# Performance work log

Hardware: AMD Instinct MI355X
Metric: run time of the kernel (lower is better)

## Reference

```python
import jax, jax.numpy as jnp
import numpy as np

EMBED = 64
HEADS = 8
DHEAD = EMBED // HEADS  # 8
LAYERS = 4
VOCAB = 32000
SEQ = 1024
BATCH = 8
EPS = 1e-5


def setup_inputs() -> dict:
    key = jax.random.key(0)
    ks = jax.random.split(key, 24)
    s = 0.02
    inp = {
        "x": jax.random.randint(ks[0], (BATCH, SEQ), 0, VOCAB),
        "targets": jax.random.randint(ks[1], (BATCH, SEQ), 0, VOCAB),
        "tok_emb": jax.random.normal(ks[2], (VOCAB, EMBED)) * s,
        "pos_emb": jax.random.normal(ks[3], (SEQ, EMBED)) * s,
        # per-layer, per-head q/k/v projections (stored as (in,out) so y = x @ W + b)
        "Wq": jax.random.normal(ks[4], (LAYERS, HEADS, EMBED, DHEAD)) * s,
        "bq": jax.random.normal(ks[5], (LAYERS, HEADS, DHEAD)) * s,
        "Wk": jax.random.normal(ks[6], (LAYERS, HEADS, EMBED, DHEAD)) * s,
        "bk": jax.random.normal(ks[7], (LAYERS, HEADS, DHEAD)) * s,
        "Wv": jax.random.normal(ks[8], (LAYERS, HEADS, EMBED, DHEAD)) * s,
        "bv": jax.random.normal(ks[9], (LAYERS, HEADS, DHEAD)) * s,
        "ln1_g": jnp.ones((LAYERS, EMBED)) + jax.random.normal(ks[10], (LAYERS, EMBED)) * s,
        "ln1_b": jax.random.normal(ks[11], (LAYERS, EMBED)) * s,
        "ln2_g": jnp.ones((LAYERS, EMBED)) + jax.random.normal(ks[12], (LAYERS, EMBED)) * s,
        "ln2_b": jax.random.normal(ks[13], (LAYERS, EMBED)) * s,
        "W1": jax.random.normal(ks[14], (LAYERS, EMBED, 4 * EMBED)) * s,
        "b1": jax.random.normal(ks[15], (LAYERS, 4 * EMBED)) * s,
        "W2": jax.random.normal(ks[16], (LAYERS, 4 * EMBED, EMBED)) * s,
        "b2": jax.random.normal(ks[17], (LAYERS, EMBED)) * s,
        "Wout": jax.random.normal(ks[18], (EMBED, VOCAB)) * s,
        "bout": jax.random.normal(ks[19], (VOCAB,)) * s,
    }
    return inp


def _layernorm(x, g, b):
    mu = jnp.mean(x, axis=-1, keepdims=True)
    var = jnp.var(x, axis=-1, keepdims=True)
    return (x - mu) / jnp.sqrt(var + EPS) * g + b


def _mha(h, Wq, bq, Wk, bk, Wv, bv):
    B, T, C = h.shape
    q = jnp.einsum('btc,hcd->bhtd', h, Wq) + bq[:, None, :]
    k = jnp.einsum('btc,hcd->bhtd', h, Wk) + bk[:, None, :]
    v = jnp.einsum('btc,hcd->bhtd', h, Wv) + bv[:, None, :]
    # FAITHFUL to source: key output is .view(B, C, T) -- a raw reshape, not transpose
    kr = k.reshape(B, HEADS, DHEAD, T)
    w = jnp.einsum('bhtd,bhds->bhts', q, kr)  # [B,H,T,T]
    w = jnp.tril(w)
    w = jnp.where(w == 0, -jnp.inf, w)
    w = jax.nn.softmax(w / np.sqrt(DHEAD), axis=-1)
    o = jnp.einsum('bhts,bhsd->bhtd', w, v)
    return o.transpose(0, 2, 1, 3).reshape(B, T, HEADS * DHEAD)


def _forward(x, targets, tok_emb, pos_emb, Wq, bq, Wk, bk, Wv, bv,
             ln1_g, ln1_b, ln2_g, ln2_b, W1, b1, W2, b2, Wout, bout):
    B, T = x.shape
    h = tok_emb[x] + pos_emb[:T]
    for l in range(LAYERS):
        h = h + _layernorm(_mha(h, Wq[l], bq[l], Wk[l], bk[l], Wv[l], bv[l]), ln1_g[l], ln1_b[l])
        z = _layernorm(h, ln2_g[l], ln2_b[l])
        h = h + jax.nn.relu(z @ W1[l] + b1[l]) @ W2[l] + b2[l]
    logits = h @ Wout + bout  # [B,T,V]
    lp = jax.nn.log_softmax(logits.reshape(B * T, -1), axis=-1)
    nll = -jnp.take_along_axis(lp, targets.reshape(B * T, 1), axis=1)
    loss = jnp.mean(nll)
    return logits, loss


def reference(x, targets, tok_emb, pos_emb, Wq, bq, Wk, bk, Wv, bv,
              ln1_g, ln1_b, ln2_g, ln2_b, W1, b1, W2, b2, Wout, bout):
    return _forward(x, targets, tok_emb, pos_emb, Wq, bq, Wk, bk, Wv, bv,
                    ln1_g, ln1_b, ln2_g, ln2_b, W1, b1, W2, b2, Wout, bout)
```

## Files before the change

kernel.cpp:

```cpp
#include <hip/hip_runtime.h>
#include <hip/hip_bf16.h>
#include <math.h>

#define BB 8
#define TT 1024
#define CC 64
#define HH 8
#define DH 8
#define NLAY 4
#define VV 32000
#define FF 256
#define NR (BB*TT)
#define NLOGIT 262144000
#define NCB 125

typedef unsigned short u16;
typedef __attribute__((ext_vector_type(8))) short short8v;
typedef __attribute__((ext_vector_type(4))) float f32x4;

__device__ __forceinline__ float b2f(u16 u){
  union { float f; unsigned int i; } c; c.i = ((unsigned int)u) << 16; return c.f;
}
__device__ __forceinline__ u16 f2b(float f){
  union { float f; unsigned int i; } c; c.f = f;
  unsigned int x = c.i;
  return (u16)((x + 0x7FFF + ((x >> 16) & 1)) >> 16);
}

__global__ void k_probe(const void* ln1g, int* flag){
  if (threadIdx.x == 0 && blockIdx.x == 0){
    const u16* p = (const u16*)ln1g;
    int cnt = 0;
    for (int i = 0; i < 256; i++){ if ((p[i] >> 8) == 0x3F) cnt++; }
    *flag = (cnt > 192) ? 1 : 0;
  }
}

struct ConvArgs {
  const void* src[18];
  float* dst[18];
  int n[18];
  int blkoff[19];
  const int* flag;
  u16* wout16;
};
__global__ void k_convert(ConvArgs a){
  int isb = *a.flag;
  int bid = blockIdx.x;
  int t = 0;
  while (bid >= a.blkoff[t + 1]) t++;
  int base = (bid - a.blkoff[t]) * 1024 + threadIdx.x;
  const u16* s16 = (const u16*)a.src[t];
  const float* s32 = (const float*)a.src[t];
  float* d = a.dst[t];
  int n = a.n[t];
  #pragma unroll
  for (int e = 0; e < 4; e++){
    int i = base + e * 256;
    if (i < n){
      float v = isb ? b2f(s16[i]) : s32[i];
      d[i] = v;
      if (t == 16) a.wout16[i] = f2b(v);
    }
  }
}

__global__ void k_embed(const int* __restrict__ x, const float* __restrict__ tok,
                        const float* __restrict__ pos, float* __restrict__ h){
  int i = blockIdx.x * 256 + threadIdx.x;
  int r = i >> 6, c = i & 63;
  int t = r & (TT - 1);
  h[i] = tok[x[r] * 64 + c] + pos[t * 64 + c];
}

__global__ void k_qkv(const float* __restrict__ h,
                      const float* __restrict__ wq, const float* __restrict__ bq,
                      const float* __restrict__ wk, const float* __restrict__ bk,
                      const float* __restrict__ wv, const float* __restrict__ bv,
                      float* __restrict__ q, float* __restrict__ kp, float* __restrict__ vv){
  __shared__ float hs[4][64];
  int tid = threadIdx.x;
  int row0 = blockIdx.x * 4;
  hs[tid >> 6][tid & 63] = h[row0 * 64 + tid];
  __syncthreads();
  int rr = tid >> 6, o = tid & 63;
  int head = o >> 3, d = o & 7;
  int row = row0 + rr;
  int b = row >> 10, t = row & (TT - 1);
  float aq = bq[head * 8 + d], ak = bk[head * 8 + d], av = bv[head * 8 + d];
  #pragma unroll
  for (int c = 0; c < 64; c++){
    float hv = hs[rr][c];
    aq += hv * wq[(head * 64 + c) * 8 + d];
    ak += hv * wk[(head * 64 + c) * 8 + d];
    av += hv * wv[(head * 64 + c) * 8 + d];
  }
  int bh = b * HH + head;
  q[(bh * TT + t) * 8 + d] = aq;
  int i = t * 8 + d;
  kp[(bh * TT + (i & 1023)) * 8 + (i >> 10)] = ak;
  vv[(bh * TT + t) * 8 + d] = av;
}

__global__ void k_attn(const float* __restrict__ q, const float* __restrict__ kp,
                       const float* __restrict__ vv, float* __restrict__ att){
  __shared__ float qs[64][8], ks[64][8], vs[64][8];
  __shared__ float2 ml[256];
  __shared__ float po[256][8];
  int tid = threadIdx.x;
  int bh = blockIdx.y;
  int t0 = blockIdx.x * 64;
  const float* qb = q + (bh * TT + t0) * 8;
  for (int idx = tid; idx < 512; idx += 256) ((float*)qs)[idx] = qb[idx];
  __syncthreads();
  int tr = tid >> 2, pp = tid & 3;
  int t = t0 + tr;
  float qr[8];
  #pragma unroll
  for (int d = 0; d < 8; d++) qr[d] = qs[tr][d];
  float m = -1e30f, l = 0.f;
  float o[8] = {0,0,0,0,0,0,0,0};
  int ntile = blockIdx.x + 1;
  for (int st = 0; st < ntile; st++){
    int s0 = st * 64;
    __syncthreads();
    const float* kb = kp + (bh * TT + s0) * 8;
    const float* vb = vv + (bh * TT + s0) * 8;
    for (int idx = tid; idx < 512; idx += 256){
      ((float*)ks)[idx] = kb[idx];
      ((float*)vs)[idx] = vb[idx];
    }
    __syncthreads();
    float sc[16];
    float tm = -1e30f;
    #pragma unroll
    for (int j = 0; j < 16; j++){
      int si = pp + j * 4;
      int s = s0 + si;
      float acc = 0.f;
      #pragma unroll
      for (int d = 0; d < 8; d++) acc += qr[d] * ks[si][d];
      sc[j] = (s <= t) ? acc * 0.35355339059327378f : -1e30f;
      tm = fmaxf(tm, sc[j]);
    }
    float mn = fmaxf(m, tm);
    float fac = __expf(m - mn);
    l *= fac;
    #pragma unroll
    for (int d = 0; d < 8; d++) o[d] *= fac;
    #pragma unroll
    for (int j = 0; j < 16; j++){
      if (sc[j] > -0.9e30f){
        float e = __expf(sc[j] - mn);
        l += e;
        int si = pp + j * 4;
        #pragma unroll
        for (int d = 0; d < 8; d++) o[d] += e * vs[si][d];
      }
    }
    m = mn;
  }
  ml[tid] = make_float2(m, l);
  #pragma unroll
  for (int d = 0; d < 8; d++) po[tid][d] = o[d];
  __syncthreads();
  if (pp == 0){
    float M = -1e30f;
    #pragma unroll
    for (int p2 = 0; p2 < 4; p2++) M = fmaxf(M, ml[tid + p2].x);
    float L = 0.f;
    float O[8] = {0,0,0,0,0,0,0,0};
    #pragma unroll
    for (int p2 = 0; p2 < 4; p2++){
      float w = __expf(ml[tid + p2].x - M);
      L += ml[tid + p2].y * w;
      #pragma unroll
      for (int d = 0; d < 8; d++) O[d] += po[tid + p2][d] * w;
    }
    float inv = 1.f / L;
    int b = bh >> 3, hh = bh & 7;
    float* op = att + (b * TT + t) * 64 + hh * 8;
    #pragma unroll
    for (int d = 0; d < 8; d++) op[d] = O[d] * inv;
  }
}

__global__ void k_lnres(const float* __restrict__ src, const float* __restrict__ g,
                        const float* __restrict__ bb, float* __restrict__ h){
  int tid = threadIdx.x;
  int row = blockIdx.x * 4 + (tid >> 6);
  int lane = tid & 63;
  float x = src[row * 64 + lane];
  float s = x, sq = x * x;
  for (int msk = 32; msk; msk >>= 1){
    s += __shfl_xor(s, msk, 64);
    sq += __shfl_xor(sq, msk, 64);
  }
  float mu = s * (1.f / 64);
  float var = sq * (1.f / 64) - mu * mu;
  float rstd = rsqrtf(fmaxf(var, 0.f) + 1e-5f);
  h[row * 64 + lane] += (x - mu) * rstd * g[lane] + bb[lane];
}

__global__ void k_ffn(float* __restrict__ h, const float* __restrict__ g, const float* __restrict__ bb,
                      const float* __restrict__ w1, const float* __restrict__ b1,
                      const float* __restrict__ w2, const float* __restrict__ b2){
  __shared__ float z[8][64];
  __shared__ float a[8][256];
  int tid = threadIdx.x;
  int row0 = blockIdx.x * 8;
  {
    int rr = tid >> 5, cp = tid & 31;
    int c0 = cp * 2;
    const float* hp = h + (row0 + rr) * 64;
    float x0 = hp[c0], x1 = hp[c0 + 1];
    float s = x0 + x1, sq = x0 * x0 + x1 * x1;
    for (int msk = 16; msk; msk >>= 1){
      s += __shfl_xor(s, msk, 64);
      sq += __shfl_xor(sq, msk, 64);
    }
    float mu = s * (1.f / 64);
    float var = sq * (1.f / 64) - mu * mu;
    float rstd = rsqrtf(fmaxf(var, 0.f) + 1e-5f);
    z[rr][c0]     = (x0 - mu) * rstd * g[c0] + bb[c0];
    z[rr][c0 + 1] = (x1 - mu) * rstd * g[c0 + 1] + bb[c0 + 1];
  }
  __syncthreads();
  {
    int j = tid;
    float acc[8];
    float bj = b1[j];
    #pragma unroll
    for (int r = 0; r < 8; r++) acc[r] = bj;
    for (int c = 0; c < 64; c++){
      float w = w1[c * 256 + j];
      #pragma unroll
      for (int r = 0; r < 8; r++) acc[r] += z[r][c] * w;
    }
    #pragma unroll
    for (int r = 0; r < 8; r++) a[r][j] = fmaxf(acc[r], 0.f);
  }
  __syncthreads();
  #pragma unroll
  for (int half = 0; half < 2; half++){
    int oi = tid + half * 256;
    int r = oi >> 6, c = oi & 63;
    float acc = b2[c];
    for (int k = 0; k < 256; k++) acc += a[r][k] * w2[k * 64 + c];
    h[(row0 + r) * 64 + c] += acc;
  }
}

__global__ void k_h2b(const float* __restrict__ h, u16* __restrict__ hb){
  int i = blockIdx.x * 256 + threadIdx.x;
  hb[i] = f2b(h[i]);
}

__global__ void __launch_bounds__(256) k_logits(const u16* __restrict__ hb, const u16* __restrict__ wb,
                                                const float* __restrict__ bout, float* __restrict__ logits,
                                                float2* __restrict__ part){
  int tid = threadIdx.x;
  int wave = tid >> 6, lane = tid & 63;
  int lr = lane & 15, lg = lane >> 4;
  int row0 = blockIdx.y * 64;
  int colw = blockIdx.x * 256 + wave * 64;

  short8v af[4][2];
  #pragma unroll
  for (int mi = 0; mi < 4; mi++)
    #pragma unroll
    for (int kk = 0; kk < 2; kk++)
      af[mi][kk] = *(const short8v*)(hb + (row0 + mi * 16 + lr) * 64 + kk * 32 + lg * 8);

  short8v bf[4][2];
  #pragma unroll
  for (int nf = 0; nf < 4; nf++){
    int col = colw + nf * 16 + lr;
    #pragma unroll
    for (int kk = 0; kk < 2; kk++){
      #pragma unroll
      for (int i = 0; i < 8; i++)
        bf[nf][kk][i] = (short)wb[(kk * 32 + lg * 8 + i) * VV + col];
    }
  }

  f32x4 acc[4][4];
  #pragma unroll
  for (int mi = 0; mi < 4; mi++)
    #pragma unroll
    for (int nf = 0; nf < 4; nf++)
      acc[mi][nf] = (f32x4){0.f, 0.f, 0.f, 0.f};

  #pragma unroll
  for (int mi = 0; mi < 4; mi++){
    #pragma unroll
    for (int nf = 0; nf < 4; nf++){
      acc[mi][nf] = __builtin_amdgcn_mfma_f32_16x16x32_bf16(af[mi][0], bf[nf][0], acc[mi][nf], 0, 0, 0);
      acc[mi][nf] = __builtin_amdgcn_mfma_f32_16x16x32_bf16(af[mi][1], bf[nf][1], acc[mi][nf], 0, 0, 0);
    }
  }

  float bo[4];
  #pragma unroll
  for (int nf = 0; nf < 4; nf++) bo[nf] = bout[colw + nf * 16 + lr];

  #pragma unroll
  for (int mi = 0; mi < 4; mi++){
    #pragma unroll
    for (int nf = 0; nf < 4; nf++){
      int colg = colw + nf * 16 + lr;
      #pragma unroll
      for (int r = 0; r < 4; r++){
        int rowg = row0 + mi * 16 + lg * 4 + r;
        logits[(size_t)rowg * VV + colg] = acc[mi][nf][r] + bo[nf];
      }
    }
  }

  __shared__ float2 wml[4][64];
  #pragma unroll
  for (int mi = 0; mi < 4; mi++){
    #pragma unroll
    for (int r = 0; r < 4; r++){
      float v0 = acc[mi][0][r] + bo[0], v1 = acc[mi][1][r] + bo[1];
      float v2 = acc[mi][2][r] + bo[2], v3 = acc[mi][3][r] + bo[3];
      float mx = fmaxf(fmaxf(v0, v1), fmaxf(v2, v3));
      for (int msk = 1; msk < 16; msk <<= 1) mx = fmaxf(mx, __shfl_xor(mx, msk, 64));
      float sume = __expf(v0 - mx) + __expf(v1 - mx) + __expf(v2 - mx) + __expf(v3 - mx);
      for (int msk = 1; msk < 16; msk <<= 1) sume += __shfl_xor(sume, msk, 64);
      if (lr == 0) wml[wave][mi * 16 + lg * 4 + r] = make_float2(mx, sume);
    }
  }
  __syncthreads();
  if (tid < 64){
    float M = -1e30f;
    #pragma unroll
    for (int w = 0; w < 4; w++) M = fmaxf(M, wml[w][tid].x);
    float L = 0.f;
    #pragma unroll
    for (int w = 0; w < 4; w++){
      float2 p = wml[w][tid];
      L += p.y * __expf(p.x - M);
    }
    part[(size_t)blockIdx.x * NR + row0 + tid] = make_float2(M, L);
  }
}

__global__ void k_loss(const float2* __restrict__ part, const float* __restrict__ logits,
                       const int* __restrict__ tgt, float* __restrict__ lpart){
  int row = blockIdx.x * 256 + threadIdx.x;
  float M = -1e30f;
  for (int j = 0; j < NCB; j++) M = fmaxf(M, part[(size_t)j * NR + row].x);
  float L = 0.f;
  for (int j = 0; j < NCB; j++){
    float2 p = part[(size_t)j * NR + row];
    L += p.y * __expf(p.x - M);
  }
  float lse = M + __logf(L);
  float tl = logits[(size_t)row * VV + tgt[row]];
  float nll = lse - tl;
  __shared__ float red[4];
  for (int msk = 32; msk; msk >>= 1) nll += __shfl_xor(nll, msk, 64);
  if ((threadIdx.x & 63) == 0) red[threadIdx.x >> 6] = nll;
  __syncthreads();
  if (threadIdx.x == 0) lpart[blockIdx.x] = red[0] + red[1] + red[2] + red[3];
}
__global__ void k_loss2(const float* __restrict__ lpart, float* __restrict__ out){
  if (threadIdx.x == 0 && blockIdx.x == 0){
    float s = 0.f;
    for (int i = 0; i < 32; i++) s += lpart[i];
    out[NLOGIT] = s * (1.f / NR);
  }
}

extern "C" void kernel_launch(void* const* d_in, const int* in_sizes, int n_in,
                              void* d_out, int out_size, void* d_ws, size_t ws_size,
                              hipStream_t stream){
  (void)in_sizes; (void)n_in; (void)out_size; (void)ws_size;
  const int* x = (const int*)d_in[0];
  const int* targets = (const int*)d_in[1];
  float* out = (float*)d_out;

  static const int WN[18] = {2048000, 65536, 16384, 256, 16384, 256, 16384, 256,
                             256, 256, 256, 256, 65536, 1024, 65536, 256, 2048000, 32000};
  char* ws = (char*)d_ws;
  size_t off = 0;
  auto alloc = [&](size_t bytes) -> void* {
    void* p = ws + off;
    off += (bytes + 255) & ~(size_t)255;
    return p;
  };
  int* flag = (int*)alloc(256);
  float* wf[18];
  for (int i = 0; i < 18; i++) wf[i] = (float*)alloc((size_t)WN[i] * 4);
  float* h     = (float*)alloc((size_t)NR * 64 * 4);
  float* q     = (float*)alloc((size_t)NR * 64 * 4);
  float* kp    = (float*)alloc((size_t)NR * 64 * 4);
  float* v     = (float*)alloc((size_t)NR * 64 * 4);
  float* att_o = (float*)alloc((size_t)NR * 64 * 4);
  u16* hb      = (u16*)alloc((size_t)NR * 64 * 2);
  u16* wout16  = (u16*)alloc((size_t)2048000 * 2);
  float2* part = (float2*)alloc((size_t)NCB * NR * 8);
  float* lpart = (float*)alloc(32 * 4);

  hipLaunchKernelGGL(k_probe, dim3(1), dim3(64), 0, stream, d_in[10], flag);
  ConvArgs ca;
  int blk = 0;
  for (int i = 0; i < 18; i++){
    ca.src[i] = d_in[2 + i];
    ca.dst[i] = wf[i];
    ca.n[i] = WN[i];
    ca.blkoff[i] = blk;
    blk += (WN[i] + 1023) / 1024;
  }
  ca.blkoff[18] = blk;
  ca.flag = flag;
  ca.wout16 = wout16;
  hipLaunchKernelGGL(k_convert, dim3(blk), dim3(256), 0, stream, ca);

  hipLaunchKernelGGL(k_embed, dim3(2048), dim3(256), 0, stream, x, wf[0], wf[1], h);

  for (int l = 0; l < NLAY; l++){
    hipLaunchKernelGGL(k_qkv, dim3(2048), dim3(256), 0, stream, h,
                       wf[2] + l * 4096, wf[3] + l * 64,
                       wf[4] + l * 4096, wf[5] + l * 64,
                       wf[6] + l * 4096, wf[7] + l * 64,
                       q, kp, v);
    hipLaunchKernelGGL(k_attn, dim3(16, 64), dim3(256), 0, stream, q, kp, v, att_o);
    hipLaunchKernelGGL(k_lnres, dim3(2048), dim3(256), 0, stream, att_o,
                       wf[8] + l * 64, wf[9] + l * 64, h);
    hipLaunchKernelGGL(k_ffn, dim3(1024), dim3(256), 0, stream, h,
                       wf[10] + l * 64, wf[11] + l * 64,
                       wf[12] + l * 16384, wf[13] + l * 256,
                       wf[14] + l * 16384, wf[15] + l * 64);
  }

  hipLaunchKernelGGL(k_h2b, dim3(2048), dim3(256), 0, stream, h, hb);
  hipLaunchKernelGGL(k_logits, dim3(NCB, 128), dim3(256), 0, stream, hb, wout16, wf[17], out, part);
  hipLaunchKernelGGL(k_loss, dim3(32), dim3(256), 0, stream, part, out, targets, lpart);
  hipLaunchKernelGGL(k_loss2, dim3(1), dim3(64), 0, stream, lpart, out);
}
```

Before: 825.2 us.

## Rewrite attention with bf16 MFMA and transpose Wout for vectorized B loads

Attention is rewritten as one-wave blocks of 16 query rows. QK^T and PV are computed with bf16 16x16x32 MFMA instructions over 32-key chunks, with an online softmax done through cross-lane shuffles. Q (pre-scaled), K and a transposed V are now stored in bf16 by the QKV kernel, which halves their memory traffic. Wout is also stored transposed in bf16, so the logits kernel loads B fragments as 16-byte vectors instead of strided scalar loads. In exchange, attention scores and probabilities lose precision in bf16, and only 8 of the 32 K dimension slots in the MFMA are used.

```diff
diff --git a/kernel.cpp b/kernel.cpp
--- a/kernel.cpp
+++ b/kernel.cpp
@@ -15,16 +15,20 @@
 #define NCB 125
 
 typedef unsigned short u16;
+typedef unsigned int u32;
 typedef __attribute__((ext_vector_type(8))) short short8v;
 typedef __attribute__((ext_vector_type(4))) float f32x4;
 
 __device__ __forceinline__ float b2f(u16 u){
-  union { float f; unsigned int i; } c; c.i = ((unsigned int)u) << 16; return c.f;
+  union { float f; u32 i; } c; c.i = ((u32)u) << 16; return c.f;
 }
 __device__ __forceinline__ u16 f2b(float f){
-  union { float f; unsigned int i; } c; c.f = f;
-  unsigned int x = c.i;
+  union { float f; u32 i; } c; c.f = f;
+  u32 x = c.i;
   return (u16)((x + 0x7FFF + ((x >> 16) & 1)) >> 16);
+}
+__device__ __forceinline__ u32 pack2(float lo, float hi){
+  return (u32)f2b(lo) | ((u32)f2b(hi) << 16);
 }
 
 __global__ void k_probe(const void* ln1g, int* flag){
@@ -42,7 +46,7 @@
   int n[18];
   int blkoff[19];
   const int* flag;
-  u16* wout16;
+  u16* wt16;
 };
 __global__ void k_convert(ConvArgs a){
   int isb = *a.flag;
@@ -60,7 +64,10 @@
     if (i < n){
       float v = isb ? b2f(s16[i]) : s32[i];
       d[i] = v;
-      if (t == 16) a.wout16[i] = f2b(v);
+      if (t == 16){
+        int k = i / VV, col = i - k * VV;
+        a.wt16[(size_t)col * 64 + k] = f2b(v);
+      }
     }
   }
 }
@@ -77,7 +84,7 @@
                       const float* __restrict__ wq, const float* __restrict__ bq,
                       const float* __restrict__ wk, const float* __restrict__ bk,
                       const float* __restrict__ wv, const float* __restrict__ bv,
-                      float* __restrict__ q, float* __restrict__ kp, float* __restrict__ vv){
+                      u16* __restrict__ q16, u16* __restrict__ kp16, u16* __restrict__ vt16){
   __shared__ float hs[4][64];
   int tid = threadIdx.x;
   int row0 = blockIdx.x * 4;
@@ -96,92 +103,104 @@
     av += hv * wv[(head * 64 + c) * 8 + d];
   }
   int bh = b * HH + head;
-  q[(bh * TT + t) * 8 + d] = aq;
+  q16[((size_t)bh * TT + t) * 8 + d] = f2b(aq * 0.35355339059327378f);
   int i = t * 8 + d;
-  kp[(bh * TT + (i & 1023)) * 8 + (i >> 10)] = ak;
-  vv[(bh * TT + t) * 8 + d] = av;
-}
-
-__global__ void k_attn(const float* __restrict__ q, const float* __restrict__ kp,
-                       const float* __restrict__ vv, float* __restrict__ att){
-  __shared__ float qs[64][8], ks[64][8], vs[64][8];
-  __shared__ float2 ml[256];
-  __shared__ float po[256][8];
-  int tid = threadIdx.x;
+  kp16[((size_t)bh * TT + (i & 1023)) * 8 + (i >> 10)] = f2b(ak);
+  vt16[((size_t)bh * 8 + d) * TT + t] = f2b(av);
+}
+
+__global__ void __launch_bounds__(64) k_attn(const u16* __restrict__ q16, const u16* __restrict__ kp16,
+                                             const u16* __restrict__ vt16, float* __restrict__ att){
+  int lane = threadIdx.x & 63;
+  int lr = lane & 15, lg = lane >> 4;
   int bh = blockIdx.y;
-  int t0 = blockIdx.x * 64;
-  const float* qb = q + (bh * TT + t0) * 8;
-  for (int idx = tid; idx < 512; idx += 256) ((float*)qs)[idx] = qb[idx];
-  __syncthreads();
-  int tr = tid >> 2, pp = tid & 3;
-  int t = t0 + tr;
-  float qr[8];
-  #pragma unroll
-  for (int d = 0; d < 8; d++) qr[d] = qs[tr][d];
+  int tb = blockIdx.x * 16;
+  int t_g = tb + lr;
+
+  short8v qf = {0,0,0,0,0,0,0,0};
+  if (lg == 0) qf = *(const short8v*)(q16 + ((size_t)bh * TT + tb + lr) * 8);
+
   float m = -1e30f, l = 0.f;
-  float o[8] = {0,0,0,0,0,0,0,0};
-  int ntile = blockIdx.x + 1;
-  for (int st = 0; st < ntile; st++){
-    int s0 = st * 64;
-    __syncthreads();
-    const float* kb = kp + (bh * TT + s0) * 8;
-    const float* vb = vv + (bh * TT + s0) * 8;
-    for (int idx = tid; idx < 512; idx += 256){
-      ((float*)ks)[idx] = kb[idx];
-      ((float*)vs)[idx] = vb[idx];
-    }
-    __syncthreads();
-    float sc[16];
-    float tm = -1e30f;
-    #pragma unroll
-    for (int j = 0; j < 16; j++){
-      int si = pp + j * 4;
-      int s = s0 + si;
-      float acc = 0.f;
+  f32x4 o = {0.f, 0.f, 0.f, 0.f};
+  int nchunk = (tb >> 5) + 1;
+
+  for (int c = 0; c < nchunk; c++){
+    int s0 = c * 32;
+    bool skipB = (s0 + 16 > tb + 15);
+    short8v kA = {0,0,0,0,0,0,0,0}, kB = {0,0,0,0,0,0,0,0};
+    if (lg == 0){
+      kA = *(const short8v*)(kp16 + ((size_t)bh * TT + s0 + lr) * 8);
+      if (!skipB) kB = *(const short8v*)(kp16 + ((size_t)bh * TT + s0 + 16 + lr) * 8);
+    }
+    f32x4 sA = __builtin_amdgcn_mfma_f32_16x16x32_bf16(kA, qf, (f32x4){0.f,0.f,0.f,0.f}, 0, 0, 0);
+    f32x4 sB;
+    if (!skipB)
+      sB = __builtin_amdgcn_mfma_f32_16x16x32_bf16(kB, qf, (f32x4){0.f,0.f,0.f,0.f}, 0, 0, 0);
+    else
+      sB = (f32x4){-1e30f, -1e30f, -1e30f, -1e30f};
+
+    if (s0 + 15 > tb){
       #pragma unroll
-      for (int d = 0; d < 8; d++) acc += qr[d] * ks[si][d];
-      sc[j] = (s <= t) ? acc * 0.35355339059327378f : -1e30f;
-      tm = fmaxf(tm, sc[j]);
-    }
+      for (int r = 0; r < 4; r++) if (s0 + lg * 4 + r > t_g) sA[r] = -1e30f;
+    }
+    if (!skipB && s0 + 31 > tb){
+      #pragma unroll
+      for (int r = 0; r < 4; r++) if (s0 + 16 + lg * 4 + r > t_g) sB[r] = -1e30f;
+    }
+
+    float tm = fmaxf(fmaxf(fmaxf(sA[0], sA[1]), fmaxf(sA[2], sA[3])),
+                     fmaxf(fmaxf(sB[0], sB[1]), fmaxf(sB[2], sB[3])));
+    tm = fmaxf(tm, __shfl_xor(tm, 16, 64));
+    tm = fmaxf(tm, __shfl_xor(tm, 32, 64));
     float mn = fmaxf(m, tm);
     float fac = __expf(m - mn);
     l *= fac;
-    #pragma unroll
-    for (int d = 0; d < 8; d++) o[d] *= fac;
-    #pragma unroll
-    for (int j = 0; j < 16; j++){
-      if (sc[j] > -0.9e30f){
-        float e = __expf(sc[j] - mn);
-        l += e;
-        int si = pp + j * 4;
-        #pragma unroll
-        for (int d = 0; d < 8; d++) o[d] += e * vs[si][d];
-      }
-    }
+    {
+      float f0 = __shfl(fac, lg * 4 + 0, 64);
+      float f1 = __shfl(fac, lg * 4 + 1, 64);
+      float f2 = __shfl(fac, lg * 4 + 2, 64);
+      float f3 = __shfl(fac, lg * 4 + 3, 64);
+      o[0] *= f0; o[1] *= f1; o[2] *= f2; o[3] *= f3;
+    }
+    f32x4 pA, pB;
+    #pragma unroll
+    for (int r = 0; r < 4; r++){ pA[r] = __expf(sA[r] - mn); pB[r] = __expf(sB[r] - mn); }
+    float ls = pA[0] + pA[1] + pA[2] + pA[3] + pB[0] + pB[1] + pB[2] + pB[3];
+    ls += __shfl_xor(ls, 16, 64);
+    ls += __shfl_xor(ls, 32, 64);
+    l += ls;
     m = mn;
-  }
-  ml[tid] = make_float2(m, l);
-  #pragma unroll
-  for (int d = 0; d < 8; d++) po[tid][d] = o[d];
-  __syncthreads();
-  if (pp == 0){
-    float M = -1e30f;
-    #pragma unroll
-    for (int p2 = 0; p2 < 4; p2++) M = fmaxf(M, ml[tid + p2].x);
-    float L = 0.f;
-    float O[8] = {0,0,0,0,0,0,0,0};
-    #pragma unroll
-    for (int p2 = 0; p2 < 4; p2++){
-      float w = __expf(ml[tid + p2].x - M);
-      L += ml[tid + p2].y * w;
-      #pragma unroll
-      for (int d = 0; d < 8; d++) O[d] += po[tid + p2][d] * w;
-    }
-    float inv = 1.f / L;
-    int b = bh >> 3, hh = bh & 7;
-    float* op = att + (b * TT + t) * 64 + hh * 8;
-    #pragma unroll
-    for (int d = 0; d < 8; d++) op[d] = O[d] * inv;
+
+    u32 a0 = pack2(pA[0], pA[1]), a1 = pack2(pA[2], pA[3]);
+    u32 b0 = pack2(pB[0], pB[1]), b1 = pack2(pB[2], pB[3]);
+    int src0 = ((2 * lg) & 3) * 16 + lr;
+    int src1 = src0 + 16;
+    u32 A0 = __shfl((int)a0, src0, 64), A1 = __shfl((int)a1, src0, 64);
+    u32 A2 = __shfl((int)a0, src1, 64), A3 = __shfl((int)a1, src1, 64);
+    u32 B0 = __shfl((int)b0, src0, 64), B1 = __shfl((int)b1, src0, 64);
+    u32 B2 = __shfl((int)b0, src1, 64), B3 = __shfl((int)b1, src1, 64);
+    union { u32 u[4]; short8v v; } pu;
+    if (lg < 2){ pu.u[0] = A0; pu.u[1] = A1; pu.u[2] = A2; pu.u[3] = A3; }
+    else       { pu.u[0] = B0; pu.u[1] = B1; pu.u[2] = B2; pu.u[3] = B3; }
+
+    short8v vf = {0,0,0,0,0,0,0,0};
+    if (lr < 8) vf = *(const short8v*)(vt16 + ((size_t)bh * 8 + lr) * TT + s0 + lg * 8);
+
+    o = __builtin_amdgcn_mfma_f32_16x16x32_bf16(pu.v, vf, o, 0, 0, 0);
+  }
+
+  float linv = 1.f / l;
+  float i0 = __shfl(linv, lg * 4 + 0, 64);
+  float i1 = __shfl(linv, lg * 4 + 1, 64);
+  float i2 = __shfl(linv, lg * 4 + 2, 64);
+  float i3 = __shfl(linv, lg * 4 + 3, 64);
+  if (lr < 8){
+    int b = bh >> 3, head = bh & 7;
+    float* op = att + ((size_t)b * TT + tb) * 64 + head * 8 + lr;
+    op[(lg * 4 + 0) * 64] = o[0] * i0;
+    op[(lg * 4 + 1) * 64] = o[1] * i1;
+    op[(lg * 4 + 2) * 64] = o[2] * i2;
+    op[(lg * 4 + 3) * 64] = o[3] * i3;
   }
 }
 
@@ -256,7 +275,7 @@
   hb[i] = f2b(h[i]);
 }
 
-__global__ void __launch_bounds__(256) k_logits(const u16* __restrict__ hb, const u16* __restrict__ wb,
+__global__ void __launch_bounds__(256) k_logits(const u16* __restrict__ hb, const u16* __restrict__ wt,
                                                 const float* __restrict__ bout, float* __restrict__ logits,
                                                 float2* __restrict__ part){
   int tid = threadIdx.x;
@@ -277,11 +296,8 @@
   for (int nf = 0; nf < 4; nf++){
     int col = colw + nf * 16 + lr;
     #pragma unroll
-    for (int kk = 0; kk < 2; kk++){
-      #pragma unroll
-      for (int i = 0; i < 8; i++)
-        bf[nf][kk][i] = (short)wb[(kk * 32 + lg * 8 + i) * VV + col];
-    }
+    for (int kk = 0; kk < 2; kk++)
+      bf[nf][kk] = *(const short8v*)(wt + (size_t)col * 64 + kk * 32 + lg * 8);
   }
 
   f32x4 acc[4][4];
@@ -394,12 +410,12 @@
   float* wf[18];
   for (int i = 0; i < 18; i++) wf[i] = (float*)alloc((size_t)WN[i] * 4);
   float* h     = (float*)alloc((size_t)NR * 64 * 4);
-  float* q     = (float*)alloc((size_t)NR * 64 * 4);
-  float* kp    = (float*)alloc((size_t)NR * 64 * 4);
-  float* v     = (float*)alloc((size_t)NR * 64 * 4);
   float* att_o = (float*)alloc((size_t)NR * 64 * 4);
+  u16* q16     = (u16*)alloc((size_t)NR * 64 * 2);
+  u16* kp16    = (u16*)alloc((size_t)NR * 64 * 2);
+  u16* vt16    = (u16*)alloc((size_t)NR * 64 * 2);
   u16* hb      = (u16*)alloc((size_t)NR * 64 * 2);
-  u16* wout16  = (u16*)alloc((size_t)2048000 * 2);
+  u16* wt16    = (u16*)alloc((size_t)2048000 * 2);
   float2* part = (float2*)alloc((size_t)NCB * NR * 8);
   float* lpart = (float*)alloc(32 * 4);
 
@@ -415,7 +431,7 @@
   }
   ca.blkoff[18] = blk;
   ca.flag = flag;
-  ca.wout16 = wout16;
+  ca.wt16 = wt16;
   hipLaunchKernelGGL(k_convert, dim3(blk), dim3(256), 0, stream, ca);
 
   hipLaunchKernelGGL(k_embed, dim3(2048), dim3(256), 0, stream, x, wf[0], wf[1], h);
@@ -425,8 +441,8 @@
                        wf[2] + l * 4096, wf[3] + l * 64,
                        wf[4] + l * 4096, wf[5] + l * 64,
                        wf[6] + l * 4096, wf[7] + l * 64,
-                       q, kp, v);
-    hipLaunchKernelGGL(k_attn, dim3(16, 64), dim3(256), 0, stream, q, kp, v, att_o);
+                       q16, kp16, vt16);
+    hipLaunchKernelGGL(k_attn, dim3(64, 64), dim3(64), 0, stream, q16, kp16, vt16, att_o);
     hipLaunchKernelGGL(k_lnres, dim3(2048), dim3(256), 0, stream, att_o,
                        wf[8] + l * 64, wf[9] + l * 64, h);
     hipLaunchKernelGGL(k_ffn, dim3(1024), dim3(256), 0, stream, h,
@@ -436,7 +452,7 @@
   }
 
   hipLaunchKernelGGL(k_h2b, dim3(2048), dim3(256), 0, stream, h, hb);
-  hipLaunchKernelGGL(k_logits, dim3(NCB, 128), dim3(256), 0, stream, hb, wout16, wf[17], out, part);
+  hipLaunchKernelGGL(k_logits, dim3(NCB, 128), dim3(256), 0, stream, hb, wt16, wf[17], out, part);
   hipLaunchKernelGGL(k_loss, dim3(32), dim3(256), 0, stream, part, out, targets, lpart);
   hipLaunchKernelGGL(k_loss2, dim3(1), dim3(64), 0, stream, lpart, out);
 }
```

Measured after the change: 792.0 us. 1.04x faster.
